# Optimization experiments

Measured on AMD Instinct MI355X. Metric: run time of the kernel, lower is better.

The kernel has to match this reference:

```python
import jax, jax.numpy as jnp
import numpy as np

N, M, K = 500000, 8, 16


def setup_inputs() -> dict:
    key = jax.random.key(0)
    kp, kq, ka, kx = jax.random.split(key, 4)
    p = jax.random.normal(kp, (N, M), dtype=jnp.float32)
    q = jax.random.normal(kq, (N, M), dtype=jnp.float32)
    # scale transitions to be contractive so the length-N recurrence is stable
    a = 0.2 * jax.random.normal(ka, (N, M, M), dtype=jnp.float32)
    x = jax.random.normal(kx, (N, K), dtype=jnp.float32)
    return {"p": p, "q": q, "a": a, "x": x}


def reference(p, q, a, x):
    # StrictLowerTriQSM.matmul: y_i = p_i @ f_i, with recurrence
    # f_{i+1} = a_i @ f_i + outer(q_i, x_i), f_0 = 0.  f has shape (M, K).
    def impl(f, data):
        qi, ai, xi = data
        return ai @ f + jnp.outer(qi, xi), f

    init = jnp.zeros((M, x.shape[1]), dtype=x.dtype)
    _, f = jax.lax.scan(impl, init, (q, a, x))  # f: (N, M, K)
    return jnp.einsum("nm,nmk->nk", p, f)
```

## Files before the change

### kernel.cpp

```cpp
#include <hip/hip_runtime.h>


#define NTOT 500000
#define CHUNK 64
#define NCHUNK 8192
#define G 4
#define NGPC 16
#define GRPSZ 64
#define NGRP 128
#define CLAMPI 499996

#define OFF_AGGA  0u
#define OFF_AGGB  524288u
#define OFF_GAGA  1572864u
#define OFF_GAGB  1581056u

#define AS1(p) ((const __attribute__((address_space(1))) void*)(p))
#define AS3(p) ((__attribute__((address_space(3))) void*)(p))
#define GLOAD_LDS16(gp, lp) __builtin_amdgcn_global_load_lds(AS1(gp), AS3(lp), 16, 0, 0)
#define GLOAD_LDS4(gp, lp)  __builtin_amdgcn_global_load_lds(AS1(gp), AS3(lp), 4, 0, 0)
#define WAIT_VM(n) asm volatile("s_waitcnt vmcnt(" #n ")" ::: "memory")

static __device__ __forceinline__ int iminc(int a, int b) { return a < b ? a : b; }

#define LOADFRAG(FR, EIDX) do {                                              \
    const float* aep_ = ablk + (EIDX) * 64;                                  \
    _Pragma("unroll") for (int mm = 0; mm < 8; ++mm) {                       \
      FR[2*mm]   = *(const float4*)(aep_ + mm * 8);                          \
      FR[2*mm+1] = *(const float4*)(aep_ + mm * 8 + 4);                      \
    }                                                                        \
  } while (0)

#define K1_BQ 1040
#define K1_BX 1176
#define K1_BUF 1480

#define K1_COMP(FR, EIDX, VBS, VAS, VBD, VAD) do {                           \
    const float xk_ = xblk[(EIDX) * 16 + ll];                                \
    const float4 q0_ = *(const float4*)(qblk + (EIDX) * 8);                  \
    const float4 q1_ = *(const float4*)(qblk + (EIDX) * 8 + 4);              \
    const float qv_[8] = {q0_.x,q0_.y,q0_.z,q0_.w,q1_.x,q1_.y,q1_.z,q1_.w};  \
    _Pragma("unroll") for (int mm = 0; mm < 8; ++mm) {                       \
      const float4 r0_ = FR[2*mm], r1_ = FR[2*mm+1];                         \
      VBD[mm] = qv_[mm] * xk_                                                \
              + r0_.x*VBS[0] + r0_.y*VBS[1] + r0_.z*VBS[2] + r0_.w*VBS[3]    \
              + r1_.x*VBS[4] + r1_.y*VBS[5] + r1_.z*VBS[6] + r1_.w*VBS[7];   \
      VAD[mm] = r0_.x*VAS[0] + r0_.y*VAS[1] + r0_.z*VAS[2] + r0_.w*VAS[3]    \
              + r1_.x*VAS[4] + r1_.y*VAS[5] + r1_.z*VAS[6] + r1_.w*VAS[7];   \
    }                                                                        \
  } while (0)

__global__ __launch_bounds__(256, 2) void k1_aggregate(
    const float* __restrict__ q, const float* __restrict__ a,
    const float* __restrict__ x, float* __restrict__ ws)
{
  __shared__ float sm[4 * 3 * K1_BUF];
  const int wv   = (int)(threadIdx.x >> 6);
  const int wave = blockIdx.x * 4 + wv;
  const int lane = (int)(threadIdx.x & 63);
  const int g    = lane >> 4;
  const int ll   = lane & 15;
  const int c    = wave * 4 + g;
  const bool hasA = ll >= 8;
  const int acol = ll & 7;

  const int cb = wave * 4;
  float* b0 = sm + wv * (3 * K1_BUF);
  float* b1 = b0 + K1_BUF;
  float* b2 = b0 + 2 * K1_BUF;

  float vB0[8], vA0[8], vB1[8], vA1[8];
#pragma unroll
  for (int m = 0; m < 8; ++m) { vB0[m] = 0.f; vA0[m] = 0.f; }
  if (hasA) vA0[acol] = 1.f;

  auto stage = [&](int gg, float* lb) {
    int b[4];
#pragma unroll
    for (int cc = 0; cc < 4; ++cc) b[cc] = iminc((cb + cc) * CHUNK + gg * G, CLAMPI);
    GLOAD_LDS16(a + (size_t)b[0] * 64u + lane * 4, lb);
    GLOAD_LDS16(a + (size_t)b[1] * 64u + lane * 4, lb + 260);
    GLOAD_LDS16(a + (size_t)b[2] * 64u + lane * 4, lb + 520);
    GLOAD_LDS16(a + (size_t)b[3] * 64u + lane * 4, lb + 780);
    GLOAD_LDS4(q + (size_t)(lane < 32 ? b[0] : b[1]) * 8u + (lane & 31), lb + K1_BQ);
    GLOAD_LDS4(q + (size_t)(lane < 32 ? b[2] : b[3]) * 8u + (lane & 31), lb + K1_BQ + 68);
    GLOAD_LDS4(x + (size_t)b[0] * 16u + lane, lb + K1_BX);
    GLOAD_LDS4(x + (size_t)b[1] * 16u + lane, lb + K1_BX + 80);
    GLOAD_LDS4(x + (size_t)b[2] * 16u + lane, lb + K1_BX + 160);
    GLOAD_LDS4(x + (size_t)b[3] * 16u + lane, lb + K1_BX + 240);
  };

  stage(0, b0);
  stage(1, b1);
#pragma unroll 1
  for (int gg = 0; gg < NGPC; ++gg) {
    float* lb = b0;
    if (gg + 2 < NGPC) {
      stage(gg + 2, b2);
      WAIT_VM(20);
    } else if (gg + 1 < NGPC) {
      WAIT_VM(10);
    } else {
      WAIT_VM(0);
    }
    const float* ablk = lb + g * 260;
    const float* qblk = lb + K1_BQ + (g >> 1) * 68 + (g & 1) * 32;
    const float* xblk = lb + K1_BX + g * 80;

    float4 A_0[16], A_1[16];
    LOADFRAG(A_0, 0);
    LOADFRAG(A_1, 1);  K1_COMP(A_0, 0, vB0, vA0, vB1, vA1);
    LOADFRAG(A_0, 2);  K1_COMP(A_1, 1, vB1, vA1, vB0, vA0);
    LOADFRAG(A_1, 3);  K1_COMP(A_0, 2, vB0, vA0, vB1, vA1);
                       K1_COMP(A_1, 3, vB1, vA1, vB0, vA0);

    float* t = b0; b0 = b1; b1 = b2; b2 = t;
  }

  {
    float* dst = ws + OFF_AGGB + (size_t)c * 128u + (size_t)ll * 8u;
#pragma unroll
    for (int m = 0; m < 8; ++m) dst[m] = vB0[m];
  }
  if (hasA) {
    float* dst = ws + OFF_AGGA + (size_t)c * 64u + (size_t)acol * 8u;
#pragma unroll
    for (int m = 0; m < 8; ++m) dst[m] = vA0[m];
  }
}

__global__ __launch_bounds__(64) void k2a_groupscan(float* __restrict__ ws)
{
  __shared__ float sA[GRPSZ * 64];
  const int g    = blockIdx.x;
  const int lane = (int)(threadIdx.x & 63);
  const bool isB = lane < 16;
  const bool isA = (lane >= 16) && (lane < 24);
  const int bcol = lane & 15;
  const int acol = (lane - 16) & 7;

#pragma unroll 1
  for (int t = 0; t < 16; ++t)
    GLOAD_LDS16(ws + OFF_AGGA + (size_t)g * (GRPSZ * 64u) + t * 256 + lane * 4,
                sA + t * 256);

  float v[8];
#pragma unroll
  for (int m = 0; m < 8; ++m) v[m] = 0.f;
  if (isA) v[acol] = 1.f;

  float4 nb0, nb1;
  {
    const float* s = ws + OFF_AGGB + (size_t)(g * GRPSZ) * 128u + (size_t)bcol * 8u;
    nb0 = *(const float4*)s; nb1 = *(const float4*)(s + 4);
  }
  WAIT_VM(0);

#pragma unroll 1
  for (int j = 0; j < GRPSZ; ++j) {
    const int c = g * GRPSZ + j;
    float bB[8] = {nb0.x, nb0.y, nb0.z, nb0.w, nb1.x, nb1.y, nb1.z, nb1.w};
    if (j + 1 < GRPSZ) {
      const float* s = ws + OFF_AGGB + (size_t)(c + 1) * 128u + (size_t)bcol * 8u;
      nb0 = *(const float4*)s; nb1 = *(const float4*)(s + 4);
    }
    if (isB) {
      float* dst = ws + OFF_AGGB + (size_t)c * 128u + (size_t)bcol * 8u;
#pragma unroll
      for (int m = 0; m < 8; ++m) dst[m] = v[m];
    } else if (isA) {
      float* dst = ws + OFF_AGGA + (size_t)c * 64u + (size_t)acol * 8u;
#pragma unroll
      for (int m = 0; m < 8; ++m) dst[m] = v[m];
    }
    const float* Aj = sA + j * 64;
    float nv[8];
#pragma unroll
    for (int m = 0; m < 8; ++m) nv[m] = 0.f;
#pragma unroll
    for (int t = 0; t < 8; ++t) {
      float4 col0 = *(const float4*)(Aj + t * 8);
      float4 col1 = *(const float4*)(Aj + t * 8 + 4);
      nv[0] += col0.x * v[t]; nv[1] += col0.y * v[t];
      nv[2] += col0.z * v[t]; nv[3] += col0.w * v[t];
      nv[4] += col1.x * v[t]; nv[5] += col1.y * v[t];
      nv[6] += col1.z * v[t]; nv[7] += col1.w * v[t];
    }
    if (isB) {
#pragma unroll
      for (int m = 0; m < 8; ++m) nv[m] += bB[m];
    }
#pragma unroll
    for (int m = 0; m < 8; ++m) v[m] = nv[m];
  }

  if (isB) {
    float* dst = ws + OFF_GAGB + (size_t)g * 128u + (size_t)bcol * 8u;
#pragma unroll
    for (int m = 0; m < 8; ++m) dst[m] = v[m];
  } else if (isA) {
    float* dst = ws + OFF_GAGA + (size_t)g * 64u + (size_t)acol * 8u;
#pragma unroll
    for (int m = 0; m < 8; ++m) dst[m] = v[m];
  }
}

__global__ __launch_bounds__(64) void k2b_topscan(float* __restrict__ ws)
{
  __shared__ float sA[NGRP * 64];
  const int lane = (int)(threadIdx.x & 63);
  const bool isB = lane < 16;
  const bool isA = (lane >= 16) && (lane < 24);
  const int bcol = lane & 15;
  const int acol = (lane - 16) & 7;

#pragma unroll 1
  for (int t = 0; t < 32; ++t)
    GLOAD_LDS16(ws + OFF_GAGA + t * 256 + lane * 4, sA + t * 256);

  float v[8];
#pragma unroll
  for (int m = 0; m < 8; ++m) v[m] = 0.f;
  if (isA) v[acol] = 1.f;

  float4 nb0, nb1;
  {
    const float* s = ws + OFF_GAGB + (size_t)bcol * 8u;
    nb0 = *(const float4*)s; nb1 = *(const float4*)(s + 4);
  }
  WAIT_VM(0);

#pragma unroll 1
  for (int j = 0; j < NGRP; ++j) {
    float bB[8] = {nb0.x, nb0.y, nb0.z, nb0.w, nb1.x, nb1.y, nb1.z, nb1.w};
    if (j + 1 < NGRP) {
      const float* s = ws + OFF_GAGB + (size_t)(j + 1) * 128u + (size_t)bcol * 8u;
      nb0 = *(const float4*)s; nb1 = *(const float4*)(s + 4);
    }
    if (isB) {
      float* dst = ws + OFF_GAGB + (size_t)j * 128u + (size_t)bcol * 8u;
#pragma unroll
      for (int m = 0; m < 8; ++m) dst[m] = v[m];
    }
    const float* Aj = sA + j * 64;
    float nv[8];
#pragma unroll
    for (int m = 0; m < 8; ++m) nv[m] = 0.f;
#pragma unroll
    for (int t = 0; t < 8; ++t) {
      float4 col0 = *(const float4*)(Aj + t * 8);
      float4 col1 = *(const float4*)(Aj + t * 8 + 4);
      nv[0] += col0.x * v[t]; nv[1] += col0.y * v[t];
      nv[2] += col0.z * v[t]; nv[3] += col0.w * v[t];
      nv[4] += col1.x * v[t]; nv[5] += col1.y * v[t];
      nv[6] += col1.z * v[t]; nv[7] += col1.w * v[t];
    }
    if (isB) {
#pragma unroll
      for (int m = 0; m < 8; ++m) nv[m] += bB[m];
    }
#pragma unroll
    for (int m = 0; m < 8; ++m) v[m] = nv[m];
  }
}

#define K3_BQ 1040
#define K3_BP 1176
#define K3_BX 1312
#define K3_BUF 1616

#define K3_COMP(FR, EIDX, FS, FD) do {                                       \
    const float xk_ = xblk[(EIDX) * 16 + k];                                 \
    const float4 q0_ = *(const float4*)(qblk + (EIDX) * 8);                  \
    const float4 q1_ = *(const float4*)(qblk + (EIDX) * 8 + 4);              \
    const float4 p0_ = *(const float4*)(pblk + (EIDX) * 8);                  \
    const float4 p1_ = *(const float4*)(pblk + (EIDX) * 8 + 4);              \
    const float y_ = p0_.x*FS[0] + p0_.y*FS[1] + p0_.z*FS[2] + p0_.w*FS[3]   \
                   + p1_.x*FS[4] + p1_.y*FS[5] + p1_.z*FS[6] + p1_.w*FS[7];  \
    const int i_ = c * CHUNK + gg * G + (EIDX);                              \
    if (i_ < NTOT) out[(size_t)i_ * 16u + k] = y_;                           \
    const float qv_[8] = {q0_.x,q0_.y,q0_.z,q0_.w,q1_.x,q1_.y,q1_.z,q1_.w};  \
    _Pragma("unroll") for (int mm = 0; mm < 8; ++mm) {                       \
      const float4 r0_ = FR[2*mm], r1_ = FR[2*mm+1];                         \
      FD[mm] = qv_[mm] * xk_                                                 \
             + r0_.x*FS[0] + r0_.y*FS[1] + r0_.z*FS[2] + r0_.w*FS[3]         \
             + r1_.x*FS[4] + r1_.y*FS[5] + r1_.z*FS[6] + r1_.w*FS[7];        \
    }                                                                        \
  } while (0)

__global__ __launch_bounds__(256, 2) void k3_output(
    const float* __restrict__ p, const float* __restrict__ q,
    const float* __restrict__ a, const float* __restrict__ x,
    const float* __restrict__ ws, float* __restrict__ out)
{
  __shared__ float sm3[4 * 3 * K3_BUF];
  const int wv   = (int)(threadIdx.x >> 6);
  const int wave = blockIdx.x * 4 + wv;
  const int lane = (int)(threadIdx.x & 63);
  const int g    = lane >> 4;
  const int k    = lane & 15;
  const int c    = wave * 4 + g;
  const int grp  = c >> 6;

  const int cb = wave * 4;
  float* b0 = sm3 + wv * (3 * K3_BUF);
  float* b1 = b0 + K3_BUF;
  float* b2 = b0 + 2 * K3_BUF;

  auto stage = [&](int gg, float* lb) {
    int b[4];
#pragma unroll
    for (int cc = 0; cc < 4; ++cc) b[cc] = iminc((cb + cc) * CHUNK + gg * G, CLAMPI);
    GLOAD_LDS16(a + (size_t)b[0] * 64u + lane * 4, lb);
    GLOAD_LDS16(a + (size_t)b[1] * 64u + lane * 4, lb + 260);
    GLOAD_LDS16(a + (size_t)b[2] * 64u + lane * 4, lb + 520);
    GLOAD_LDS16(a + (size_t)b[3] * 64u + lane * 4, lb + 780);
    GLOAD_LDS4(q + (size_t)(lane < 32 ? b[0] : b[1]) * 8u + (lane & 31), lb + K3_BQ);
    GLOAD_LDS4(q + (size_t)(lane < 32 ? b[2] : b[3]) * 8u + (lane & 31), lb + K3_BQ + 68);
    GLOAD_LDS4(p + (size_t)(lane < 32 ? b[0] : b[1]) * 8u + (lane & 31), lb + K3_BP);
    GLOAD_LDS4(p + (size_t)(lane < 32 ? b[2] : b[3]) * 8u + (lane & 31), lb + K3_BP + 68);
    GLOAD_LDS4(x + (size_t)b[0] * 16u + lane, lb + K3_BX);
    GLOAD_LDS4(x + (size_t)b[1] * 16u + lane, lb + K3_BX + 80);
    GLOAD_LDS4(x + (size_t)b[2] * 16u + lane, lb + K3_BX + 160);
    GLOAD_LDS4(x + (size_t)b[3] * 16u + lane, lb + K3_BX + 240);
  };

  stage(0, b0);
  stage(1, b1);

  const float* __restrict__ pA  = ws + OFF_AGGA + (size_t)c * 64u;
  const float* __restrict__ gBp = ws + OFF_GAGB + (size_t)grp * 128u + (size_t)k * 8u;
  const float* __restrict__ lBp = ws + OFF_AGGB + (size_t)c * 128u + (size_t)k * 8u;
  float gcol[8];
#pragma unroll
  for (int t = 0; t < 8; ++t) gcol[t] = gBp[t];
  float f0[8], f1[8];
#pragma unroll
  for (int m = 0; m < 8; ++m) f0[m] = lBp[m];
#pragma unroll
  for (int t = 0; t < 8; ++t) {
    float4 col0 = *(const float4*)(pA + t * 8);
    float4 col1 = *(const float4*)(pA + t * 8 + 4);
    const float gt = gcol[t];
    f0[0] += col0.x * gt; f0[1] += col0.y * gt;
    f0[2] += col0.z * gt; f0[3] += col0.w * gt;
    f0[4] += col1.x * gt; f0[5] += col1.y * gt;
    f0[6] += col1.z * gt; f0[7] += col1.w * gt;
  }

#pragma unroll 1
  for (int gg = 0; gg < NGPC; ++gg) {
    float* lb = b0;
    if (gg + 2 < NGPC) {
      stage(gg + 2, b2);
      WAIT_VM(24);
    } else if (gg + 1 < NGPC) {
      WAIT_VM(12);
    } else {
      WAIT_VM(0);
    }
    const float* ablk = lb + g * 260;
    const float* qblk = lb + K3_BQ + (g >> 1) * 68 + (g & 1) * 32;
    const float* pblk = lb + K3_BP + (g >> 1) * 68 + (g & 1) * 32;
    const float* xblk = lb + K3_BX + g * 80;

    float4 A_0[16], A_1[16];
    LOADFRAG(A_0, 0);
    LOADFRAG(A_1, 1);  K3_COMP(A_0, 0, f0, f1);
    LOADFRAG(A_0, 2);  K3_COMP(A_1, 1, f1, f0);
    LOADFRAG(A_1, 3);  K3_COMP(A_0, 2, f0, f1);
                       K3_COMP(A_1, 3, f1, f0);

    float* t = b0; b0 = b1; b1 = b2; b2 = t;
  }
}

extern "C" void kernel_launch(void* const* d_in, const int* in_sizes, int n_in,
                              void* d_out, int out_size, void* d_ws, size_t ws_size,
                              hipStream_t stream)
{
  const float* p = (const float*)d_in[0];
  const float* q = (const float*)d_in[1];
  const float* a = (const float*)d_in[2];
  const float* x = (const float*)d_in[3];
  float* out = (float*)d_out;
  float* ws  = (float*)d_ws;

  hipLaunchKernelGGL(k1_aggregate, dim3(NCHUNK / 4 / 4), dim3(256), 0, stream, q, a, x, ws);
  hipLaunchKernelGGL(k2a_groupscan, dim3(NGRP), dim3(64), 0, stream, ws);
  hipLaunchKernelGGL(k2b_topscan, dim3(1), dim3(64), 0, stream, ws);
  hipLaunchKernelGGL(k3_output, dim3(NCHUNK / 4 / 4), dim3(256), 0, stream, p, q, a, x, ws, out);
}
```

Before: 187.2 us.

## Use smaller chunks, three-level scan, and direct LDS reads for more parallelism

Cuts the chunk length from 64 to 32 when the workspace allows, giving 16384 chunks. The chunk-level scan gains a third level (group, supergroup, top) so the serial top scan stays short. The kernels stage two timesteps per iteration instead of four and read A rows directly from LDS rather than through register fragments. Launch bounds rise to 4 blocks per CU. The aim is to shorten the per-wave serial recurrence and raise occupancy, at the cost of more workspace traffic and an extra scan launch.

```diff
diff --git a/kernel.cpp b/kernel.cpp
--- a/kernel.cpp
+++ b/kernel.cpp
@@ -2,18 +2,6 @@
 
 
 #define NTOT 500000
-#define CHUNK 64
-#define NCHUNK 8192
-#define G 4
-#define NGPC 16
-#define GRPSZ 64
-#define NGRP 128
-#define CLAMPI 499996
-
-#define OFF_AGGA  0u
-#define OFF_AGGB  524288u
-#define OFF_GAGA  1572864u
-#define OFF_GAGB  1581056u
 
 #define AS1(p) ((const __attribute__((address_space(1))) void*)(p))
 #define AS3(p) ((__attribute__((address_space(3))) void*)(p))
@@ -23,25 +11,28 @@
 
 static __device__ __forceinline__ int iminc(int a, int b) { return a < b ? a : b; }
 
-#define LOADFRAG(FR, EIDX) do {                                              \
-    const float* aep_ = ablk + (EIDX) * 64;                                  \
-    _Pragma("unroll") for (int mm = 0; mm < 8; ++mm) {                       \
-      FR[2*mm]   = *(const float4*)(aep_ + mm * 8);                          \
-      FR[2*mm+1] = *(const float4*)(aep_ + mm * 8 + 4);                      \
-    }                                                                        \
-  } while (0)
-
-#define K1_BQ 1040
-#define K1_BX 1176
-#define K1_BUF 1480
-
-#define K1_COMP(FR, EIDX, VBS, VAS, VBD, VAD) do {                           \
-    const float xk_ = xblk[(EIDX) * 16 + ll];                                \
-    const float4 q0_ = *(const float4*)(qblk + (EIDX) * 8);                  \
-    const float4 q1_ = *(const float4*)(qblk + (EIDX) * 8 + 4);              \
+template<int NC> struct P {
+  static constexpr int CH   = (NC == 16384) ? 32 : 64;
+  static constexpr int NST  = CH / 2;
+  static constexpr int NG   = NC / 64;
+  static constexpr int NS   = NG / 64;
+  static constexpr int AGGA = 0;
+  static constexpr int AGGB = NC * 64;
+  static constexpr int GAGA = NC * 192;
+  static constexpr int GAGB = NC * 192 + NG * 64;
+  static constexpr int SGA  = NC * 192 + NG * 192;
+  static constexpr int SGB  = NC * 192 + NG * 192 + NS * 64;
+  static constexpr size_t BYTES = (size_t)(NC * 192 + NG * 192 + NS * 192) * 4u;
+};
+
+#define K1_COMP(E, VBS, VAS, VBD, VAD) do {                                  \
+    const float xk_ = xgb[(E) * 16];                                         \
+    const float4 q0_ = *(const float4*)(qgb + (E) * 8);                      \
+    const float4 q1_ = *(const float4*)(qgb + (E) * 8 + 4);                  \
     const float qv_[8] = {q0_.x,q0_.y,q0_.z,q0_.w,q1_.x,q1_.y,q1_.z,q1_.w};  \
     _Pragma("unroll") for (int mm = 0; mm < 8; ++mm) {                       \
-      const float4 r0_ = FR[2*mm], r1_ = FR[2*mm+1];                         \
+      const float4 r0_ = *(const float4*)(agb + (E) * 256 + mm * 8);         \
+      const float4 r1_ = *(const float4*)(agb + (E) * 256 + mm * 8 + 4);     \
       VBD[mm] = qv_[mm] * xk_                                                \
               + r0_.x*VBS[0] + r0_.y*VBS[1] + r0_.z*VBS[2] + r0_.w*VBS[3]    \
               + r1_.x*VBS[4] + r1_.y*VBS[5] + r1_.z*VBS[6] + r1_.w*VBS[7];   \
@@ -50,11 +41,14 @@
     }                                                                        \
   } while (0)
 
-__global__ __launch_bounds__(256, 2) void k1_aggregate(
+template<int NC>
+__global__ __launch_bounds__(256, 4) void k1_aggregate(
     const float* __restrict__ q, const float* __restrict__ a,
     const float* __restrict__ x, float* __restrict__ ws)
 {
-  __shared__ float sm[4 * 3 * K1_BUF];
+  using PP = P<NC>;
+  constexpr int CH = PP::CH, NST = PP::NST;
+  __shared__ float sm[4 * 3 * 704];
   const int wv   = (int)(threadIdx.x >> 6);
   const int wave = blockIdx.x * 4 + wv;
   const int lane = (int)(threadIdx.x & 63);
@@ -62,76 +56,74 @@
   const int ll   = lane & 15;
   const int c    = wave * 4 + g;
   const bool hasA = ll >= 8;
-  const int acol = ll & 7;
+  const int acol  = ll & 7;
 
   const int cb = wave * 4;
-  float* b0 = sm + wv * (3 * K1_BUF);
-  float* b1 = b0 + K1_BUF;
-  float* b2 = b0 + 2 * K1_BUF;
+  float* b0 = sm + wv * 2112;
+  float* b1 = b0 + 704;
+  float* b2 = b0 + 1408;
+
+  const int goff = g * 64;
+  const int qoff = 512 + g * 16;
+  const int xoff = 576 + (g >> 1) * 64 + (g & 1) * 32 + ll;
 
   float vB0[8], vA0[8], vB1[8], vA1[8];
 #pragma unroll
   for (int m = 0; m < 8; ++m) { vB0[m] = 0.f; vA0[m] = 0.f; }
   if (hasA) vA0[acol] = 1.f;
 
-  auto stage = [&](int gg, float* lb) {
-    int b[4];
-#pragma unroll
-    for (int cc = 0; cc < 4; ++cc) b[cc] = iminc((cb + cc) * CHUNK + gg * G, CLAMPI);
-    GLOAD_LDS16(a + (size_t)b[0] * 64u + lane * 4, lb);
-    GLOAD_LDS16(a + (size_t)b[1] * 64u + lane * 4, lb + 260);
-    GLOAD_LDS16(a + (size_t)b[2] * 64u + lane * 4, lb + 520);
-    GLOAD_LDS16(a + (size_t)b[3] * 64u + lane * 4, lb + 780);
-    GLOAD_LDS4(q + (size_t)(lane < 32 ? b[0] : b[1]) * 8u + (lane & 31), lb + K1_BQ);
-    GLOAD_LDS4(q + (size_t)(lane < 32 ? b[2] : b[3]) * 8u + (lane & 31), lb + K1_BQ + 68);
-    GLOAD_LDS4(x + (size_t)b[0] * 16u + lane, lb + K1_BX);
-    GLOAD_LDS4(x + (size_t)b[1] * 16u + lane, lb + K1_BX + 80);
-    GLOAD_LDS4(x + (size_t)b[2] * 16u + lane, lb + K1_BX + 160);
-    GLOAD_LDS4(x + (size_t)b[3] * 16u + lane, lb + K1_BX + 240);
+  const int gl = lane >> 4, ql = lane & 15;
+  auto stage = [&](int ss, float* lb) {
+    const int base = cb * CH + ss * 2;
+    GLOAD_LDS16(a + (size_t)iminc(base + gl * CH,     NTOT - 1) * 64u + ql * 4, lb);
+    GLOAD_LDS16(a + (size_t)iminc(base + gl * CH + 1, NTOT - 1) * 64u + ql * 4, lb + 256);
+    GLOAD_LDS4 (q + (size_t)iminc(base + (lane >> 4) * CH + ((lane >> 3) & 1), NTOT - 1) * 8u  + (lane & 7),  lb + 512);
+    GLOAD_LDS4 (x + (size_t)iminc(base + (lane >> 5) * CH + ((lane >> 4) & 1), NTOT - 1) * 16u + (lane & 15), lb + 576);
+    GLOAD_LDS4 (x + (size_t)iminc(base + (2 + (lane >> 5)) * CH + ((lane >> 4) & 1), NTOT - 1) * 16u + (lane & 15), lb + 640);
   };
 
   stage(0, b0);
   stage(1, b1);
 #pragma unroll 1
-  for (int gg = 0; gg < NGPC; ++gg) {
+  for (int ss = 0; ss < NST; ++ss) {
     float* lb = b0;
-    if (gg + 2 < NGPC) {
-      stage(gg + 2, b2);
-      WAIT_VM(20);
-    } else if (gg + 1 < NGPC) {
+    if (ss + 2 < NST) {
+      stage(ss + 2, b2);
       WAIT_VM(10);
+    } else if (ss + 1 < NST) {
+      WAIT_VM(5);
     } else {
       WAIT_VM(0);
     }
-    const float* ablk = lb + g * 260;
-    const float* qblk = lb + K1_BQ + (g >> 1) * 68 + (g & 1) * 32;
-    const float* xblk = lb + K1_BX + g * 80;
-
-    float4 A_0[16], A_1[16];
-    LOADFRAG(A_0, 0);
-    LOADFRAG(A_1, 1);  K1_COMP(A_0, 0, vB0, vA0, vB1, vA1);
-    LOADFRAG(A_0, 2);  K1_COMP(A_1, 1, vB1, vA1, vB0, vA0);
-    LOADFRAG(A_1, 3);  K1_COMP(A_0, 2, vB0, vA0, vB1, vA1);
-                       K1_COMP(A_1, 3, vB1, vA1, vB0, vA0);
-
+    const float* agb = lb + goff;
+    const float* qgb = lb + qoff;
+    const float* xgb = lb + xoff;
+    K1_COMP(0, vB0, vA0, vB1, vA1);
+    K1_COMP(1, vB1, vA1, vB0, vA0);
     float* t = b0; b0 = b1; b1 = b2; b2 = t;
   }
 
   {
-    float* dst = ws + OFF_AGGB + (size_t)c * 128u + (size_t)ll * 8u;
+    float* dst = ws + PP::AGGB + (size_t)c * 128u + (size_t)ll * 8u;
 #pragma unroll
     for (int m = 0; m < 8; ++m) dst[m] = vB0[m];
   }
   if (hasA) {
-    float* dst = ws + OFF_AGGA + (size_t)c * 64u + (size_t)acol * 8u;
+    float* dst = ws + PP::AGGA + (size_t)c * 64u + (size_t)acol * 8u;
 #pragma unroll
     for (int m = 0; m < 8; ++m) dst[m] = vA0[m];
   }
 }
 
-__global__ __launch_bounds__(64) void k2a_groupscan(float* __restrict__ ws)
-{
-  __shared__ float sA[GRPSZ * 64];
+template<int NC, int LV>
+__global__ __launch_bounds__(64) void k2scan(float* __restrict__ ws)
+{
+  using PP = P<NC>;
+  constexpr int OFFAIN  = (LV == 0) ? PP::AGGA : PP::GAGA;
+  constexpr int OFFBIN  = (LV == 0) ? PP::AGGB : PP::GAGB;
+  constexpr int OFFAOUT = (LV == 0) ? PP::GAGA : PP::SGA;
+  constexpr int OFFBOUT = (LV == 0) ? PP::GAGB : PP::SGB;
+  __shared__ float sA[64 * 64];
   const int g    = blockIdx.x;
   const int lane = (int)(threadIdx.x & 63);
   const bool isB = lane < 16;
@@ -141,8 +133,7 @@
 
 #pragma unroll 1
   for (int t = 0; t < 16; ++t)
-    GLOAD_LDS16(ws + OFF_AGGA + (size_t)g * (GRPSZ * 64u) + t * 256 + lane * 4,
-                sA + t * 256);
+    GLOAD_LDS16(ws + OFFAIN + (size_t)g * 4096u + t * 256 + lane * 4, sA + t * 256);
 
   float v[8];
 #pragma unroll
@@ -151,25 +142,25 @@
 
   float4 nb0, nb1;
   {
-    const float* s = ws + OFF_AGGB + (size_t)(g * GRPSZ) * 128u + (size_t)bcol * 8u;
+    const float* s = ws + OFFBIN + (size_t)(g * 64) * 128u + (size_t)bcol * 8u;
     nb0 = *(const float4*)s; nb1 = *(const float4*)(s + 4);
   }
   WAIT_VM(0);
 
 #pragma unroll 1
-  for (int j = 0; j < GRPSZ; ++j) {
-    const int c = g * GRPSZ + j;
+  for (int j = 0; j < 64; ++j) {
+    const int c = g * 64 + j;
     float bB[8] = {nb0.x, nb0.y, nb0.z, nb0.w, nb1.x, nb1.y, nb1.z, nb1.w};
-    if (j + 1 < GRPSZ) {
-      const float* s = ws + OFF_AGGB + (size_t)(c + 1) * 128u + (size_t)bcol * 8u;
+    if (j + 1 < 64) {
+      const float* s = ws + OFFBIN + (size_t)(c + 1) * 128u + (size_t)bcol * 8u;
       nb0 = *(const float4*)s; nb1 = *(const float4*)(s + 4);
     }
     if (isB) {
-      float* dst = ws + OFF_AGGB + (size_t)c * 128u + (size_t)bcol * 8u;
+      float* dst = ws + OFFBIN + (size_t)c * 128u + (size_t)bcol * 8u;
 #pragma unroll
       for (int m = 0; m < 8; ++m) dst[m] = v[m];
     } else if (isA) {
-      float* dst = ws + OFF_AGGA + (size_t)c * 64u + (size_t)acol * 8u;
+      float* dst = ws + OFFAIN + (size_t)c * 64u + (size_t)acol * 8u;
 #pragma unroll
       for (int m = 0; m < 8; ++m) dst[m] = v[m];
     }
@@ -195,54 +186,40 @@
   }
 
   if (isB) {
-    float* dst = ws + OFF_GAGB + (size_t)g * 128u + (size_t)bcol * 8u;
+    float* dst = ws + OFFBOUT + (size_t)g * 128u + (size_t)bcol * 8u;
 #pragma unroll
     for (int m = 0; m < 8; ++m) dst[m] = v[m];
   } else if (isA) {
-    float* dst = ws + OFF_GAGA + (size_t)g * 64u + (size_t)acol * 8u;
+    float* dst = ws + OFFAOUT + (size_t)g * 64u + (size_t)acol * 8u;
 #pragma unroll
     for (int m = 0; m < 8; ++m) dst[m] = v[m];
   }
 }
 
-__global__ __launch_bounds__(64) void k2b_topscan(float* __restrict__ ws)
-{
-  __shared__ float sA[NGRP * 64];
+template<int NC>
+__global__ __launch_bounds__(64) void k2c_topscan(float* __restrict__ ws)
+{
+  using PP = P<NC>;
   const int lane = (int)(threadIdx.x & 63);
   const bool isB = lane < 16;
-  const bool isA = (lane >= 16) && (lane < 24);
   const int bcol = lane & 15;
-  const int acol = (lane - 16) & 7;
-
-#pragma unroll 1
-  for (int t = 0; t < 32; ++t)
-    GLOAD_LDS16(ws + OFF_GAGA + t * 256 + lane * 4, sA + t * 256);
 
   float v[8];
 #pragma unroll
   for (int m = 0; m < 8; ++m) v[m] = 0.f;
-  if (isA) v[acol] = 1.f;
-
-  float4 nb0, nb1;
-  {
-    const float* s = ws + OFF_GAGB + (size_t)bcol * 8u;
-    nb0 = *(const float4*)s; nb1 = *(const float4*)(s + 4);
-  }
-  WAIT_VM(0);
-
-#pragma unroll 1
-  for (int j = 0; j < NGRP; ++j) {
-    float bB[8] = {nb0.x, nb0.y, nb0.z, nb0.w, nb1.x, nb1.y, nb1.z, nb1.w};
-    if (j + 1 < NGRP) {
-      const float* s = ws + OFF_GAGB + (size_t)(j + 1) * 128u + (size_t)bcol * 8u;
-      nb0 = *(const float4*)s; nb1 = *(const float4*)(s + 4);
-    }
+
+#pragma unroll 1
+  for (int j = 0; j < PP::NS; ++j) {
+    float bB[8];
     if (isB) {
-      float* dst = ws + OFF_GAGB + (size_t)j * 128u + (size_t)bcol * 8u;
+      const float* s = ws + PP::SGB + (size_t)j * 128u + (size_t)bcol * 8u;
+#pragma unroll
+      for (int m = 0; m < 8; ++m) bB[m] = s[m];
+      float* dst = ws + PP::SGB + (size_t)j * 128u + (size_t)bcol * 8u;
 #pragma unroll
       for (int m = 0; m < 8; ++m) dst[m] = v[m];
     }
-    const float* Aj = sA + j * 64;
+    const float* Aj = ws + PP::SGA + (size_t)j * 64u;
     float nv[8];
 #pragma unroll
     for (int m = 0; m < 8; ++m) nv[m] = 0.f;
@@ -264,115 +241,126 @@
   }
 }
 
-#define K3_BQ 1040
-#define K3_BP 1176
-#define K3_BX 1312
-#define K3_BUF 1616
-
-#define K3_COMP(FR, EIDX, FS, FD) do {                                       \
-    const float xk_ = xblk[(EIDX) * 16 + k];                                 \
-    const float4 q0_ = *(const float4*)(qblk + (EIDX) * 8);                  \
-    const float4 q1_ = *(const float4*)(qblk + (EIDX) * 8 + 4);              \
-    const float4 p0_ = *(const float4*)(pblk + (EIDX) * 8);                  \
-    const float4 p1_ = *(const float4*)(pblk + (EIDX) * 8 + 4);              \
+#define K3_COMP(E, FS, FD) do {                                              \
+    const float xk_ = xgb[(E) * 16];                                         \
+    const float4 q0_ = *(const float4*)(qgb + (E) * 8);                      \
+    const float4 q1_ = *(const float4*)(qgb + (E) * 8 + 4);                  \
+    const float4 p0_ = *(const float4*)(pgb + (E) * 8);                      \
+    const float4 p1_ = *(const float4*)(pgb + (E) * 8 + 4);                  \
     const float y_ = p0_.x*FS[0] + p0_.y*FS[1] + p0_.z*FS[2] + p0_.w*FS[3]   \
                    + p1_.x*FS[4] + p1_.y*FS[5] + p1_.z*FS[6] + p1_.w*FS[7];  \
-    const int i_ = c * CHUNK + gg * G + (EIDX);                              \
+    const int i_ = c * CH + ss * 2 + (E);                                    \
     if (i_ < NTOT) out[(size_t)i_ * 16u + k] = y_;                           \
     const float qv_[8] = {q0_.x,q0_.y,q0_.z,q0_.w,q1_.x,q1_.y,q1_.z,q1_.w};  \
     _Pragma("unroll") for (int mm = 0; mm < 8; ++mm) {                       \
-      const float4 r0_ = FR[2*mm], r1_ = FR[2*mm+1];                         \
+      const float4 r0_ = *(const float4*)(agb + (E) * 256 + mm * 8);         \
+      const float4 r1_ = *(const float4*)(agb + (E) * 256 + mm * 8 + 4);     \
       FD[mm] = qv_[mm] * xk_                                                 \
              + r0_.x*FS[0] + r0_.y*FS[1] + r0_.z*FS[2] + r0_.w*FS[3]         \
              + r1_.x*FS[4] + r1_.y*FS[5] + r1_.z*FS[6] + r1_.w*FS[7];        \
     }                                                                        \
   } while (0)
 
-__global__ __launch_bounds__(256, 2) void k3_output(
+template<int NC>
+__global__ __launch_bounds__(256, 4) void k3_output(
     const float* __restrict__ p, const float* __restrict__ q,
     const float* __restrict__ a, const float* __restrict__ x,
     const float* __restrict__ ws, float* __restrict__ out)
 {
-  __shared__ float sm3[4 * 3 * K3_BUF];
+  using PP = P<NC>;
+  constexpr int CH = PP::CH, NST = PP::NST;
+  __shared__ float sm3[4 * 3 * 768];
   const int wv   = (int)(threadIdx.x >> 6);
   const int wave = blockIdx.x * 4 + wv;
   const int lane = (int)(threadIdx.x & 63);
   const int g    = lane >> 4;
   const int k    = lane & 15;
   const int c    = wave * 4 + g;
-  const int grp  = c >> 6;
+  const int gr   = c >> 6;
+  const int sidx = gr >> 6;
 
   const int cb = wave * 4;
-  float* b0 = sm3 + wv * (3 * K3_BUF);
-  float* b1 = b0 + K3_BUF;
-  float* b2 = b0 + 2 * K3_BUF;
-
-  auto stage = [&](int gg, float* lb) {
-    int b[4];
-#pragma unroll
-    for (int cc = 0; cc < 4; ++cc) b[cc] = iminc((cb + cc) * CHUNK + gg * G, CLAMPI);
-    GLOAD_LDS16(a + (size_t)b[0] * 64u + lane * 4, lb);
-    GLOAD_LDS16(a + (size_t)b[1] * 64u + lane * 4, lb + 260);
-    GLOAD_LDS16(a + (size_t)b[2] * 64u + lane * 4, lb + 520);
-    GLOAD_LDS16(a + (size_t)b[3] * 64u + lane * 4, lb + 780);
-    GLOAD_LDS4(q + (size_t)(lane < 32 ? b[0] : b[1]) * 8u + (lane & 31), lb + K3_BQ);
-    GLOAD_LDS4(q + (size_t)(lane < 32 ? b[2] : b[3]) * 8u + (lane & 31), lb + K3_BQ + 68);
-    GLOAD_LDS4(p + (size_t)(lane < 32 ? b[0] : b[1]) * 8u + (lane & 31), lb + K3_BP);
-    GLOAD_LDS4(p + (size_t)(lane < 32 ? b[2] : b[3]) * 8u + (lane & 31), lb + K3_BP + 68);
-    GLOAD_LDS4(x + (size_t)b[0] * 16u + lane, lb + K3_BX);
-    GLOAD_LDS4(x + (size_t)b[1] * 16u + lane, lb + K3_BX + 80);
-    GLOAD_LDS4(x + (size_t)b[2] * 16u + lane, lb + K3_BX + 160);
-    GLOAD_LDS4(x + (size_t)b[3] * 16u + lane, lb + K3_BX + 240);
+  float* b0 = sm3 + wv * 2304;
+  float* b1 = b0 + 768;
+  float* b2 = b0 + 1536;
+
+  const int goff = g * 64;
+  const int qoff = 512 + g * 16;
+  const int poff = 576 + g * 16;
+  const int xoff = 640 + (g >> 1) * 64 + (g & 1) * 32 + k;
+
+  auto stage = [&](int ss, float* lb) {
+    const int base = cb * CH + ss * 2;
+    GLOAD_LDS16(a + (size_t)iminc(base + (lane >> 4) * CH,     NTOT - 1) * 64u + (lane & 15) * 4, lb);
+    GLOAD_LDS16(a + (size_t)iminc(base + (lane >> 4) * CH + 1, NTOT - 1) * 64u + (lane & 15) * 4, lb + 256);
+    GLOAD_LDS4 (q + (size_t)iminc(base + (lane >> 4) * CH + ((lane >> 3) & 1), NTOT - 1) * 8u  + (lane & 7),  lb + 512);
+    GLOAD_LDS4 (p + (size_t)iminc(base + (lane >> 4) * CH + ((lane >> 3) & 1), NTOT - 1) * 8u  + (lane & 7),  lb + 576);
+    GLOAD_LDS4 (x + (size_t)iminc(base + (lane >> 5) * CH + ((lane >> 4) & 1), NTOT - 1) * 16u + (lane & 15), lb + 640);
+    GLOAD_LDS4 (x + (size_t)iminc(base + (2 + (lane >> 5)) * CH + ((lane >> 4) & 1), NTOT - 1) * 16u + (lane & 15), lb + 704);
   };
 
   stage(0, b0);
   stage(1, b1);
 
-  const float* __restrict__ pA  = ws + OFF_AGGA + (size_t)c * 64u;
-  const float* __restrict__ gBp = ws + OFF_GAGB + (size_t)grp * 128u + (size_t)k * 8u;
-  const float* __restrict__ lBp = ws + OFF_AGGB + (size_t)c * 128u + (size_t)k * 8u;
-  float gcol[8];
-#pragma unroll
-  for (int t = 0; t < 8; ++t) gcol[t] = gBp[t];
+  const float* __restrict__ sBc = ws + PP::SGB  + (size_t)sidx * 128u + (size_t)k * 8u;
+  const float* __restrict__ gBc = ws + PP::GAGB + (size_t)gr   * 128u + (size_t)k * 8u;
+  const float* __restrict__ gA  = ws + PP::GAGA + (size_t)gr   * 64u;
+  const float* __restrict__ pA  = ws + PP::AGGA + (size_t)c    * 64u;
+  const float* __restrict__ lBc = ws + PP::AGGB + (size_t)c    * 128u + (size_t)k * 8u;
+  float t1[8];
+#pragma unroll
+  for (int m = 0; m < 8; ++m) t1[m] = gBc[m];
+#pragma unroll
+  for (int t = 0; t < 8; ++t) {
+    float4 c0 = *(const float4*)(gA + t * 8);
+    float4 c1 = *(const float4*)(gA + t * 8 + 4);
+    const float st = sBc[t];
+    t1[0] += c0.x * st; t1[1] += c0.y * st; t1[2] += c0.z * st; t1[3] += c0.w * st;
+    t1[4] += c1.x * st; t1[5] += c1.y * st; t1[6] += c1.z * st; t1[7] += c1.w * st;
+  }
   float f0[8], f1[8];
 #pragma unroll
-  for (int m = 0; m < 8; ++m) f0[m] = lBp[m];
+  for (int m = 0; m < 8; ++m) f0[m] = lBc[m];
 #pragma unroll
   for (int t = 0; t < 8; ++t) {
-    float4 col0 = *(const float4*)(pA + t * 8);
-    float4 col1 = *(const float4*)(pA + t * 8 + 4);
-    const float gt = gcol[t];
-    f0[0] += col0.x * gt; f0[1] += col0.y * gt;
-    f0[2] += col0.z * gt; f0[3] += col0.w * gt;
-    f0[4] += col1.x * gt; f0[5] += col1.y * gt;
-    f0[6] += col1.z * gt; f0[7] += col1.w * gt;
-  }
-
-#pragma unroll 1
-  for (int gg = 0; gg < NGPC; ++gg) {
+    float4 c0 = *(const float4*)(pA + t * 8);
+    float4 c1 = *(const float4*)(pA + t * 8 + 4);
+    const float gt = t1[t];
+    f0[0] += c0.x * gt; f0[1] += c0.y * gt; f0[2] += c0.z * gt; f0[3] += c0.w * gt;
+    f0[4] += c1.x * gt; f0[5] += c1.y * gt; f0[6] += c1.z * gt; f0[7] += c1.w * gt;
+  }
+
+#pragma unroll 1
+  for (int ss = 0; ss < NST; ++ss) {
     float* lb = b0;
-    if (gg + 2 < NGPC) {
-      stage(gg + 2, b2);
-      WAIT_VM(24);
-    } else if (gg + 1 < NGPC) {
+    if (ss + 2 < NST) {
+      stage(ss + 2, b2);
       WAIT_VM(12);
+    } else if (ss + 1 < NST) {
+      WAIT_VM(6);
     } else {
       WAIT_VM(0);
     }
-    const float* ablk = lb + g * 260;
-    const float* qblk = lb + K3_BQ + (g >> 1) * 68 + (g & 1) * 32;
-    const float* pblk = lb + K3_BP + (g >> 1) * 68 + (g & 1) * 32;
-    const float* xblk = lb + K3_BX + g * 80;
-
-    float4 A_0[16], A_1[16];
-    LOADFRAG(A_0, 0);
-    LOADFRAG(A_1, 1);  K3_COMP(A_0, 0, f0, f1);
-    LOADFRAG(A_0, 2);  K3_COMP(A_1, 1, f1, f0);
-    LOADFRAG(A_1, 3);  K3_COMP(A_0, 2, f0, f1);
-                       K3_COMP(A_1, 3, f1, f0);
-
+    const float* agb = lb + goff;
+    const float* qgb = lb + qoff;
+    const float* pgb = lb + poff;
+    const float* xgb = lb + xoff;
+    K3_COMP(0, f0, f1);
+    K3_COMP(1, f1, f0);
     float* t = b0; b0 = b1; b1 = b2; b2 = t;
   }
+}
+
+template<int NC>
+static void launch_all(const float* p, const float* q, const float* a,
+                       const float* x, float* out, float* ws, hipStream_t stream)
+{
+  using PP = P<NC>;
+  hipLaunchKernelGGL(HIP_KERNEL_NAME(k1_aggregate<NC>), dim3(NC / 16), dim3(256), 0, stream, q, a, x, ws);
+  hipLaunchKernelGGL(HIP_KERNEL_NAME(k2scan<NC, 0>),    dim3(PP::NG),  dim3(64),  0, stream, ws);
+  hipLaunchKernelGGL(HIP_KERNEL_NAME(k2scan<NC, 1>),    dim3(PP::NS),  dim3(64),  0, stream, ws);
+  hipLaunchKernelGGL(HIP_KERNEL_NAME(k2c_topscan<NC>),  dim3(1),       dim3(64),  0, stream, ws);
+  hipLaunchKernelGGL(HIP_KERNEL_NAME(k3_output<NC>),    dim3(NC / 16), dim3(256), 0, stream, p, q, a, x, ws, out);
 }
 
 extern "C" void kernel_launch(void* const* d_in, const int* in_sizes, int n_in,
@@ -386,8 +374,9 @@
   float* out = (float*)d_out;
   float* ws  = (float*)d_ws;
 
-  hipLaunchKernelGGL(k1_aggregate, dim3(NCHUNK / 4 / 4), dim3(256), 0, stream, q, a, x, ws);
-  hipLaunchKernelGGL(k2a_groupscan, dim3(NGRP), dim3(64), 0, stream, ws);
-  hipLaunchKernelGGL(k2b_topscan, dim3(1), dim3(64), 0, stream, ws);
-  hipLaunchKernelGGL(k3_output, dim3(NCHUNK / 4 / 4), dim3(256), 0, stream, p, q, a, x, ws, out);
-}
+  if (ws_size >= P<16384>::BYTES) {
+    launch_all<16384>(p, q, a, x, out, ws, stream);
+  } else {
+    launch_all<8192>(p, q, a, x, out, ws, stream);
+  }
+}
```

Result: faster. 157.8 us, median of 3 (-15.7%).
